# Kernel tuning notes

Measured on AMD Instinct MI355X. Metric: run time of the kernel, lower is better.

The kernel has to match this reference:

```python
import jax, jax.numpy as jnp
import numpy as np

BATCH, SEQ, H_IN, N_STATE, H_OUT = 16, 4096, 128, 256, 128
RMIN, RMAX, MAX_PHASE = 0.9, 1.0, 6.283


def setup_inputs() -> dict:
    key = jax.random.key(0)
    ks = jax.random.split(key, 9)
    u = jax.random.normal(ks[0], (BATCH, SEQ, H_IN), jnp.float32)
    # LRU exponential parameterization init (matches torch __init__)
    u1 = jax.random.uniform(ks[1], (N_STATE,), jnp.float32)
    u2 = jax.random.uniform(ks[2], (N_STATE,), jnp.float32)
    nu_log = jnp.log(-0.5 * jnp.log(u1 * (RMAX + RMIN) * (RMAX - RMIN) + RMIN ** 2))
    theta_log = jnp.log(MAX_PHASE * u2)
    lam_abs = jnp.exp(-jnp.exp(nu_log))
    gamma_log = jnp.log(jnp.sqrt(1.0 - lam_abs ** 2))
    s2in = np.sqrt(2.0 * H_IN).astype(np.float32)
    B_re = jax.random.normal(ks[3], (N_STATE, H_IN), jnp.float32) / s2in
    B_im = jax.random.normal(ks[4], (N_STATE, H_IN), jnp.float32) / s2in
    sst = np.sqrt(float(N_STATE)).astype(np.float32)
    C_re = jax.random.normal(ks[5], (H_OUT, N_STATE), jnp.float32) / sst
    C_im = jax.random.normal(ks[6], (H_OUT, N_STATE), jnp.float32) / sst
    D = jax.random.normal(ks[7], (H_OUT, H_IN), jnp.float32) / np.sqrt(float(H_IN)).astype(np.float32)
    return dict(u=u, nu_log=nu_log, theta_log=theta_log, gamma_log=gamma_log,
                B_re=B_re, B_im=B_im, C_re=C_re, C_im=C_im, D=D)


def _combine(a, b):
    # complex affine composition: (l, x) o (l', x') -> (l*l', l'*x + x')
    l1r, l1i, x1r, x1i = a
    l2r, l2i, x2r, x2i = b
    lr = l1r * l2r - l1i * l2i
    li = l1r * l2i + l1i * l2r
    xr = l2r * x1r - l2i * x1i + x2r
    xi = l2r * x1i + l2i * x1r + x2i
    return (lr, li, xr, xi)


def reference(u, nu_log, theta_log, gamma_log, B_re, B_im, C_re, C_im, D):
    lam_mod = jnp.exp(-jnp.exp(nu_log))          # |lambda|, [N]
    th = jnp.exp(theta_log)
    lam_re = lam_mod * jnp.cos(th)
    lam_im = lam_mod * jnp.sin(th)
    gammas = jnp.exp(gamma_log)                  # [N]
    # input projection Bu_t = gamma * (B @ u_t), complex -> real/imag parts
    Bu_re = jnp.einsum('blh,nh->bln', u, B_re) * gammas  # [B,L,N]
    Bu_im = jnp.einsum('blh,nh->bln', u, B_im) * gammas
    Bsz, L, N = Bu_re.shape
    lr = jnp.broadcast_to(lam_re, (Bsz, L, N))
    li = jnp.broadcast_to(lam_im, (Bsz, L, N))
    # parallel scan of x_t = lambda * x_{t-1} + Bu_t, x0 = 0
    _, _, xr, xi = jax.lax.associative_scan(_combine, (lr, li, Bu_re, Bu_im), axis=1)
    zero = jnp.zeros((Bsz, 1, N), u.dtype)
    pre_re = jnp.concatenate([zero, xr[:, :-1]], axis=1)  # states[:, :-1]
    pre_im = jnp.concatenate([zero, xi[:, :-1]], axis=1)
    # y_t = Re(C x_{t-1}) + D u_t
    y = (jnp.einsum('bln,on->blo', pre_re, C_re)
         - jnp.einsum('bln,on->blo', pre_im, C_im)
         + jnp.einsum('blh,oh->blo', u, D))
    return y
```

## Files before the change

### kernel.cpp

```cpp
#include <hip/hip_runtime.h>
#include <math.h>

#define BATCH 16
#define SEQ   4096
#define HIN   128
#define NST   256
#define HOUT  128
#define CL    32
#define NC    (SEQ/CL)
#define ROWS  (BATCH*SEQ)
#define KTOT  640
#define NPRE  512
#define NBU   512

typedef __attribute__((ext_vector_type(8))) short short8;
typedef __attribute__((ext_vector_type(4))) float f32x4;

__device__ inline unsigned short f2bf(float f) {
  union { float f; unsigned u; } v; v.f = f;
  unsigned r = v.u + 0x7FFFu + ((v.u >> 16) & 1u);
  return (unsigned short)(r >> 16);
}
__device__ inline float bf2f(unsigned short s) {
  union { unsigned u; float f; } v; v.u = ((unsigned)s) << 16;
  return v.f;
}

__global__ __launch_bounds__(256) void k_prep(
    const float* __restrict__ nu_log, const float* __restrict__ theta_log,
    const float* __restrict__ gamma_log,
    const float* __restrict__ Bre, const float* __restrict__ Bim,
    const float* __restrict__ Cre, const float* __restrict__ Cim,
    const float* __restrict__ Dm,
    float* __restrict__ lamre, float* __restrict__ lamim,
    unsigned short* __restrict__ Wb, unsigned short* __restrict__ W) {
  int idx = blockIdx.x*256 + threadIdx.x;
  if (idx < NST) {
    float lm = expf(-expf(nu_log[idx]));
    float th = expf(theta_log[idx]);
    lamre[idx] = lm * cosf(th);
    lamim[idx] = lm * sinf(th);
  }
  if (idx < 512*HIN) {
    int r = idx >> 7, h = idx & 127;
    int g = r >> 7;
    int w = r & 127;
    int n = g*64 + (w & 63);
    float gm = expf(gamma_log[n]);
    float v = (w < 64) ? Bre[n*HIN + h] : Bim[n*HIN + h];
    Wb[idx] = f2bf(gm * v);
  }
  if (idx < HOUT*KTOT) {
    int o = idx / KTOT, k = idx - o*KTOT;
    float v;
    if (k < NST)        v =  Cre[o*NST + k];
    else if (k < 2*NST) v = -Cim[o*NST + (k - NST)];
    else                v =  Dm[o*HIN + (k - 2*NST)];
    W[idx] = f2bf(v);
  }
}

__global__ __launch_bounds__(256) void k_cast(
    const float* __restrict__ u, unsigned short* __restrict__ ubf) {
  size_t i = (size_t)(blockIdx.x*256 + threadIdx.x) * 4;
  float4 v = *(const float4*)(u + i);
  ushort4 o;
  o.x = f2bf(v.x); o.y = f2bf(v.y); o.z = f2bf(v.z); o.w = f2bf(v.w);
  *(ushort4*)(ubf + i) = o;
}

union SharedBu {
  unsigned short B[128][136];
  float stg[2][32][132];
};
__global__ __launch_bounds__(256) void k_bu(
    const unsigned short* __restrict__ ubf, const unsigned short* __restrict__ Wb,
    const float* __restrict__ lamre, const float* __restrict__ lamim,
    unsigned short* __restrict__ bu16,
    float* __restrict__ S_re, float* __restrict__ S_im) {
  __shared__ unsigned short Asl[128][136];
  __shared__ SharedBu sh;
  int tid = threadIdx.x;
  int row0 = blockIdx.x * 128;
  int wid = tid >> 6, lane = tid & 63;
  int lm = lane & 15, lq = lane >> 4;
  int m0 = (wid >> 1) * 64, n0 = (wid & 1) * 64;
  int b = row0 >> 12;
  int cbase = (row0 & 4095) >> 5;
#pragma unroll
  for (int cc = 0; cc < 8; ++cc) {
    int ch = cc*256 + tid;
    int r = ch >> 4, h0 = (ch & 15) * 8;
    *(short8*)&Asl[r][h0] = *(const short8*)&ubf[(size_t)(row0 + r)*HIN + h0];
  }
  for (int g = 0; g < 4; ++g) {
    __syncthreads();
#pragma unroll
    for (int cc = 0; cc < 8; ++cc) {
      int ch = cc*256 + tid;
      int r = ch >> 4, h0 = (ch & 15) * 8;
      *(short8*)&sh.B[r][h0] = *(const short8*)&Wb[(size_t)(g*128 + r)*HIN + h0];
    }
    __syncthreads();
    f32x4 acc[4][4];
#pragma unroll
    for (int i = 0; i < 4; ++i)
#pragma unroll
      for (int j = 0; j < 4; ++j) acc[i][j] = (f32x4)0.f;
#pragma unroll
    for (int ks = 0; ks < 4; ++ks) {
      int k0 = ks*32 + lq*8;
      short8 a[4], bb[4];
#pragma unroll
      for (int i = 0; i < 4; ++i) a[i] = *(const short8*)&Asl[m0 + i*16 + lm][k0];
#pragma unroll
      for (int j = 0; j < 4; ++j) bb[j] = *(const short8*)&sh.B[n0 + j*16 + lm][k0];
#pragma unroll
      for (int i = 0; i < 4; ++i)
#pragma unroll
        for (int j = 0; j < 4; ++j)
          acc[i][j] = __builtin_amdgcn_mfma_f32_16x16x32_bf16(a[i], bb[j], acc[i][j], 0, 0, 0);
    }
#pragma unroll
    for (int i = 0; i < 4; ++i)
#pragma unroll
      for (int j = 0; j < 4; ++j)
#pragma unroll
        for (int r = 0; r < 4; ++r)
          bu16[(size_t)(row0 + m0 + i*16 + lq*4 + r)*NBU + g*128 + n0 + j*16 + lm] =
              f2bf(acc[i][j][r]);
    for (int p = 0; p < 2; ++p) {
      __syncthreads();
#pragma unroll
      for (int ii = 0; ii < 2; ++ii) {
        int i = 2*p + ii;
#pragma unroll
        for (int j = 0; j < 4; ++j)
#pragma unroll
          for (int r = 0; r < 4; ++r) {
            int trow = ii*16 + lq*4 + r;
            sh.stg[wid >> 1][trow][n0 + j*16 + lm] = acc[i][j][r];
          }
      }
      __syncthreads();
      if (tid < 128) {
        int buf = tid >> 6, nl = tid & 63;
        int ng = g*64 + nl;
        float lr = lamre[ng], li = lamim[ng];
        float sr = 0.f, si = 0.f;
#pragma unroll
        for (int t = 0; t < 32; ++t) {
          float br = sh.stg[buf][t][nl];
          float bi = sh.stg[buf][t][64 + nl];
          float nr = lr*sr - li*si + br;
          float ni = lr*si + li*sr + bi;
          sr = nr; si = ni;
        }
        int c = cbase + buf*2 + p;
        int idx = (b*NC + c)*NST + ng;
        S_re[idx] = sr; S_im[idx] = si;
      }
    }
  }
}

__global__ __launch_bounds__(256) void k_carry2(
    const float* __restrict__ S_re, const float* __restrict__ S_im,
    const float* __restrict__ lamre, const float* __restrict__ lamim,
    float* __restrict__ G_re, float* __restrict__ G_im) {
  int blk = blockIdx.x;
  int b = blk >> 3, g = blk & 7;
  int n = threadIdx.x;
  float ar = lamre[n], ai = lamim[n];
#pragma unroll
  for (int s = 0; s < 5; ++s) { float nr = ar*ar - ai*ai, ni = 2.f*ar*ai; ar = nr; ai = ni; }
  float tr = 0.f, ti = 0.f;
#pragma unroll
  for (int cc = 0; cc < 16; ++cc) {
    int idx = (b*NC + g*16 + cc)*NST + n;
    float nr = ar*tr - ai*ti + S_re[idx];
    float ni = ar*ti + ai*tr + S_im[idx];
    tr = nr; ti = ni;
  }
  int gi = (b*8 + g)*NST + n;
  G_re[gi] = tr; G_im[gi] = ti;
}

__global__ __launch_bounds__(256) void k_final(
    const float* __restrict__ S_re, const float* __restrict__ S_im,
    const float* __restrict__ G_re, const float* __restrict__ G_im,
    const float* __restrict__ lamre, const float* __restrict__ lamim,
    float* __restrict__ X0_re, float* __restrict__ X0_im) {
  int blk = blockIdx.x;
  int b = blk >> 3, g = blk & 7;
  int n = threadIdx.x;
  float ar = lamre[n], ai = lamim[n];
#pragma unroll
  for (int s = 0; s < 5; ++s) { float nr = ar*ar - ai*ai, ni = 2.f*ar*ai; ar = nr; ai = ni; }
  float a5r = ar, a5i = ai;
#pragma unroll
  for (int s = 0; s < 4; ++s) { float nr = a5r*a5r - a5i*a5i, ni = 2.f*a5r*a5i; a5r = nr; a5i = ni; }
  float pr = 0.f, pi = 0.f;
  for (int j = 0; j < g; ++j) {
    int gi = (b*8 + j)*NST + n;
    float nr = a5r*pr - a5i*pi + G_re[gi];
    float ni = a5r*pi + a5i*pr + G_im[gi];
    pr = nr; pi = ni;
  }
  float xr = pr, xi = pi;
#pragma unroll
  for (int cc = 0; cc < 16; ++cc) {
    int idx = (b*NC + g*16 + cc)*NST + n;
    X0_re[idx] = xr; X0_im[idx] = xi;
    float nr = ar*xr - ai*xi + S_re[idx];
    float ni = ar*xi + ai*xr + S_im[idx];
    xr = nr; xi = ni;
  }
}

__global__ __launch_bounds__(256) void k_scan(
    const unsigned short* __restrict__ bu16,
    const float* __restrict__ X0_re, const float* __restrict__ X0_im,
    const float* __restrict__ lamre, const float* __restrict__ lamim,
    unsigned short* __restrict__ pre16) {
  int blk = blockIdx.x;
  int b = blk >> 7, c = blk & (NC-1);
  int tid = threadIdx.x;
  int t0 = c*CL;
  size_t rowbase = (size_t)(b*SEQ + t0);
  int n = tid;
  int gg = n >> 6, nl = n & 63;
  int cre = gg*128 + nl, cim = cre + 64;
  const unsigned short* bup = bu16 + rowbase*NBU;
  unsigned short rbr[CL], rbi[CL];
#pragma unroll
  for (int t = 0; t < CL; ++t) {
    rbr[t] = bup[(size_t)t*NBU + cre];
    rbi[t] = bup[(size_t)t*NBU + cim];
  }
  float lr = lamre[n], li = lamim[n];
  int idx = (b*NC + c)*NST + n;
  float xr = X0_re[idx], xi = X0_im[idx];
  unsigned short* pdst = pre16 + rowbase*NPRE;
#pragma unroll
  for (int t = 0; t < CL; ++t) {
    pdst[n]       = f2bf(xr);
    pdst[NST + n] = f2bf(xi);
    float br = bf2f(rbr[t]);
    float bi = bf2f(rbi[t]);
    float nr = lr*xr - li*xi + br;
    float ni = lr*xi + li*xr + bi;
    xr = nr; xi = ni; pdst += NPRE;
  }
}

__global__ __launch_bounds__(256) void k_out2(
    const unsigned short* __restrict__ pre16, const unsigned short* __restrict__ ubf,
    const unsigned short* __restrict__ W, float* __restrict__ y) {
  __shared__ unsigned short Asl[128][136];
  __shared__ unsigned short Bsl[128][136];
  int tid = threadIdx.x;
  int row0 = blockIdx.x * 128;
  int wid = tid >> 6, lane = tid & 63;
  int lm = lane & 15, lq = lane >> 4;
  int m0 = (wid >> 1) * 64, n0 = (wid & 1) * 64;
  f32x4 acc[4][4];
#pragma unroll
  for (int i = 0; i < 4; ++i)
#pragma unroll
    for (int j = 0; j < 4; ++j) acc[i][j] = (f32x4)0.f;
  for (int s = 0; s < 5; ++s) {
#pragma unroll
    for (int cc = 0; cc < 8; ++cc) {
      int ch = cc*256 + tid;
      int r = ch >> 4, h0 = (ch & 15) * 8;
      if (s < 4)
        *(short8*)&Asl[r][h0] = *(const short8*)&pre16[(size_t)(row0 + r)*NPRE + s*128 + h0];
      else
        *(short8*)&Asl[r][h0] = *(const short8*)&ubf[(size_t)(row0 + r)*HIN + h0];
      *(short8*)&Bsl[r][h0] = *(const short8*)&W[(size_t)r*KTOT + s*128 + h0];
    }
    __syncthreads();
#pragma unroll
    for (int ks = 0; ks < 4; ++ks) {
      int k0 = ks*32 + lq*8;
      short8 a[4], bb[4];
#pragma unroll
      for (int i = 0; i < 4; ++i) a[i] = *(const short8*)&Asl[m0 + i*16 + lm][k0];
#pragma unroll
      for (int j = 0; j < 4; ++j) bb[j] = *(const short8*)&Bsl[n0 + j*16 + lm][k0];
#pragma unroll
      for (int i = 0; i < 4; ++i)
#pragma unroll
        for (int j = 0; j < 4; ++j)
          acc[i][j] = __builtin_amdgcn_mfma_f32_16x16x32_bf16(a[i], bb[j], acc[i][j], 0, 0, 0);
    }
    __syncthreads();
  }
#pragma unroll
  for (int i = 0; i < 4; ++i)
#pragma unroll
    for (int j = 0; j < 4; ++j)
#pragma unroll
      for (int r = 0; r < 4; ++r)
        y[(size_t)(row0 + m0 + i*16 + lq*4 + r)*HOUT + n0 + j*16 + lm] = acc[i][j][r];
}

extern "C" void kernel_launch(void* const* d_in, const int* in_sizes, int n_in,
                              void* d_out, int out_size, void* d_ws, size_t ws_size,
                              hipStream_t stream) {
  const float* u         = (const float*)d_in[0];
  const float* nu_log    = (const float*)d_in[1];
  const float* theta_log = (const float*)d_in[2];
  const float* gamma_log = (const float*)d_in[3];
  const float* B_re      = (const float*)d_in[4];
  const float* B_im      = (const float*)d_in[5];
  const float* C_re      = (const float*)d_in[6];
  const float* C_im      = (const float*)d_in[7];
  const float* Dm        = (const float*)d_in[8];
  float* y = (float*)d_out;
  char* ws = (char*)d_ws;

  float*          lamre = (float*)(ws);
  float*          lamim = (float*)(ws + 1024);
  unsigned short* ubf   = (unsigned short*)(ws + 4096);
  unsigned short* Wb    = (unsigned short*)(ws + 4096 + 16777216);
  unsigned short* W     = (unsigned short*)(ws + 4096 + 16777216 + 131072);
  unsigned short* bu16  = (unsigned short*)(ws + 4096 + 16777216 + 131072 + 163840);
  char* pp = ws + 4096 + 16777216 + 131072 + 163840 + (size_t)ROWS*NBU*2;
  unsigned short* pre16 = (unsigned short*)pp;
  char* p2 = pp + (size_t)ROWS*NPRE*2;
  float* S_re  = (float*)(p2);
  float* S_im  = (float*)(p2 + 2097152);
  float* G_re  = (float*)(p2 + 2*2097152);
  float* G_im  = (float*)(p2 + 2*2097152 + 131072);
  float* X0_re = (float*)(p2 + 2*2097152 + 2*131072);
  float* X0_im = (float*)(p2 + 3*2097152 + 2*131072);

  k_prep<<<320, 256, 0, stream>>>(nu_log, theta_log, gamma_log, B_re, B_im,
                                  C_re, C_im, Dm, lamre, lamim, Wb, W);
  k_cast<<<(ROWS*HIN)/1024, 256, 0, stream>>>(u, ubf);
  k_bu<<<ROWS/128, 256, 0, stream>>>(ubf, Wb, lamre, lamim, bu16, S_re, S_im);
  k_carry2<<<BATCH*8, 256, 0, stream>>>(S_re, S_im, lamre, lamim, G_re, G_im);
  k_final<<<BATCH*8, 256, 0, stream>>>(S_re, S_im, G_re, G_im, lamre, lamim,
                                       X0_re, X0_im);
  k_scan<<<BATCH*NC, 256, 0, stream>>>(bu16, X0_re, X0_im, lamre, lamim, pre16);
  k_out2<<<ROWS/128, 256, 0, stream>>>(pre16, ubf, W, y);
}
```

Baseline: 187.9 us.

## Fuse chunk-local scan into Bu GEMM and apply carry correction in output GEMM

The chunk-local scan states (starting from zero) are now written as bf16 directly from the Bu GEMM kernel, which removes the bu16 buffer and the separate k_scan kernel. The output GEMM adds the carry term lambda^j * X0 while loading its A tile, using a precomputed table of lambda powers built in k_prep. This saves one full read and write of a large intermediate plus one kernel launch. In exchange, the output GEMM's load path does more global loads and arithmetic, and k_bu issues scattered 2-byte stores from only 128 threads.

```diff
diff --git a/kernel.cpp b/kernel.cpp
--- a/kernel.cpp
+++ b/kernel.cpp
@@ -11,7 +11,6 @@
 #define ROWS  (BATCH*SEQ)
 #define KTOT  640
 #define NPRE  512
-#define NBU   512
 
 typedef __attribute__((ext_vector_type(8))) short short8;
 typedef __attribute__((ext_vector_type(4))) float f32x4;
@@ -33,13 +32,22 @@
     const float* __restrict__ Cre, const float* __restrict__ Cim,
     const float* __restrict__ Dm,
     float* __restrict__ lamre, float* __restrict__ lamim,
+    float* __restrict__ lamPowRe, float* __restrict__ lamPowIm,
     unsigned short* __restrict__ Wb, unsigned short* __restrict__ W) {
   int idx = blockIdx.x*256 + threadIdx.x;
   if (idx < NST) {
     float lm = expf(-expf(nu_log[idx]));
     float th = expf(theta_log[idx]);
-    lamre[idx] = lm * cosf(th);
-    lamim[idx] = lm * sinf(th);
+    float lr = lm * cosf(th), li = lm * sinf(th);
+    lamre[idx] = lr; lamim[idx] = li;
+    float pr = 1.f, pi = 0.f;
+    for (int j = 0; j < CL; ++j) {
+      lamPowRe[j*NST + idx] = pr;
+      lamPowIm[j*NST + idx] = pi;
+      float nr = pr*lr - pi*li;
+      float ni = pr*li + pi*lr;
+      pr = nr; pi = ni;
+    }
   }
   if (idx < 512*HIN) {
     int r = idx >> 7, h = idx & 127;
@@ -76,7 +84,7 @@
 __global__ __launch_bounds__(256) void k_bu(
     const unsigned short* __restrict__ ubf, const unsigned short* __restrict__ Wb,
     const float* __restrict__ lamre, const float* __restrict__ lamim,
-    unsigned short* __restrict__ bu16,
+    unsigned short* __restrict__ preL,
     float* __restrict__ S_re, float* __restrict__ S_im) {
   __shared__ unsigned short Asl[128][136];
   __shared__ SharedBu sh;
@@ -121,14 +129,6 @@
         for (int j = 0; j < 4; ++j)
           acc[i][j] = __builtin_amdgcn_mfma_f32_16x16x32_bf16(a[i], bb[j], acc[i][j], 0, 0, 0);
     }
-#pragma unroll
-    for (int i = 0; i < 4; ++i)
-#pragma unroll
-      for (int j = 0; j < 4; ++j)
-#pragma unroll
-        for (int r = 0; r < 4; ++r)
-          bu16[(size_t)(row0 + m0 + i*16 + lq*4 + r)*NBU + g*128 + n0 + j*16 + lm] =
-              f2bf(acc[i][j][r]);
     for (int p = 0; p < 2; ++p) {
       __syncthreads();
 #pragma unroll
@@ -147,14 +147,22 @@
         int buf = tid >> 6, nl = tid & 63;
         int ng = g*64 + nl;
         float lr = lamre[ng], li = lamim[ng];
+        float rr[CL], ri[CL];
+#pragma unroll
+        for (int t = 0; t < CL; ++t) {
+          rr[t] = sh.stg[buf][t][nl];
+          ri[t] = sh.stg[buf][t][64 + nl];
+        }
+        int rowb = row0 + buf*64 + p*32;
+        unsigned short* pl = preL + (size_t)rowb*NPRE;
         float sr = 0.f, si = 0.f;
 #pragma unroll
-        for (int t = 0; t < 32; ++t) {
-          float br = sh.stg[buf][t][nl];
-          float bi = sh.stg[buf][t][64 + nl];
-          float nr = lr*sr - li*si + br;
-          float ni = lr*si + li*sr + bi;
-          sr = nr; si = ni;
+        for (int t = 0; t < CL; ++t) {
+          pl[ng]       = f2bf(sr);
+          pl[NST + ng] = f2bf(si);
+          float nr = lr*sr - li*si + rr[t];
+          float ni = lr*si + li*sr + ri[t];
+          sr = nr; si = ni; pl += NPRE;
         }
         int c = cbase + buf*2 + p;
         int idx = (b*NC + c)*NST + ng;
@@ -218,45 +226,12 @@
   }
 }
 
-__global__ __launch_bounds__(256) void k_scan(
-    const unsigned short* __restrict__ bu16,
+__global__ __launch_bounds__(256) void k_out2(
+    const unsigned short* __restrict__ preL, const unsigned short* __restrict__ ubf,
+    const unsigned short* __restrict__ W,
+    const float* __restrict__ lamPowRe, const float* __restrict__ lamPowIm,
     const float* __restrict__ X0_re, const float* __restrict__ X0_im,
-    const float* __restrict__ lamre, const float* __restrict__ lamim,
-    unsigned short* __restrict__ pre16) {
-  int blk = blockIdx.x;
-  int b = blk >> 7, c = blk & (NC-1);
-  int tid = threadIdx.x;
-  int t0 = c*CL;
-  size_t rowbase = (size_t)(b*SEQ + t0);
-  int n = tid;
-  int gg = n >> 6, nl = n & 63;
-  int cre = gg*128 + nl, cim = cre + 64;
-  const unsigned short* bup = bu16 + rowbase*NBU;
-  unsigned short rbr[CL], rbi[CL];
-#pragma unroll
-  for (int t = 0; t < CL; ++t) {
-    rbr[t] = bup[(size_t)t*NBU + cre];
-    rbi[t] = bup[(size_t)t*NBU + cim];
-  }
-  float lr = lamre[n], li = lamim[n];
-  int idx = (b*NC + c)*NST + n;
-  float xr = X0_re[idx], xi = X0_im[idx];
-  unsigned short* pdst = pre16 + rowbase*NPRE;
-#pragma unroll
-  for (int t = 0; t < CL; ++t) {
-    pdst[n]       = f2bf(xr);
-    pdst[NST + n] = f2bf(xi);
-    float br = bf2f(rbr[t]);
-    float bi = bf2f(rbi[t]);
-    float nr = lr*xr - li*xi + br;
-    float ni = lr*xi + li*xr + bi;
-    xr = nr; xi = ni; pdst += NPRE;
-  }
-}
-
-__global__ __launch_bounds__(256) void k_out2(
-    const unsigned short* __restrict__ pre16, const unsigned short* __restrict__ ubf,
-    const unsigned short* __restrict__ W, float* __restrict__ y) {
+    float* __restrict__ y) {
   __shared__ unsigned short Asl[128][136];
   __shared__ unsigned short Bsl[128][136];
   int tid = threadIdx.x;
@@ -274,10 +249,32 @@
     for (int cc = 0; cc < 8; ++cc) {
       int ch = cc*256 + tid;
       int r = ch >> 4, h0 = (ch & 15) * 8;
-      if (s < 4)
-        *(short8*)&Asl[r][h0] = *(const short8*)&pre16[(size_t)(row0 + r)*NPRE + s*128 + h0];
-      else
+      if (s < 4) {
+        int row = row0 + r;
+        int j = row & 31, cidx = row >> 5;
+        int n = ((s & 1) << 7) + h0;
+        short8 loc = *(const short8*)&preL[(size_t)row*NPRE + s*128 + h0];
+        float lre[8], lim_[8], x0r[8], x0i[8];
+        *(float4*)&lre[0]  = *(const float4*)&lamPowRe[j*NST + n];
+        *(float4*)&lre[4]  = *(const float4*)&lamPowRe[j*NST + n + 4];
+        *(float4*)&lim_[0] = *(const float4*)&lamPowIm[j*NST + n];
+        *(float4*)&lim_[4] = *(const float4*)&lamPowIm[j*NST + n + 4];
+        *(float4*)&x0r[0]  = *(const float4*)&X0_re[cidx*NST + n];
+        *(float4*)&x0r[4]  = *(const float4*)&X0_re[cidx*NST + n + 4];
+        *(float4*)&x0i[0]  = *(const float4*)&X0_im[cidx*NST + n];
+        *(float4*)&x0i[4]  = *(const float4*)&X0_im[cidx*NST + n + 4];
+        unsigned short o[8];
+#pragma unroll
+        for (int e = 0; e < 8; ++e) {
+          float lv = bf2f((unsigned short)loc[e]);
+          float v = (s < 2) ? (lv + lre[e]*x0r[e] - lim_[e]*x0i[e])
+                            : (lv + lre[e]*x0i[e] + lim_[e]*x0r[e]);
+          o[e] = f2bf(v);
+        }
+        *(short8*)&Asl[r][h0] = *(const short8*)o;
+      } else {
         *(short8*)&Asl[r][h0] = *(const short8*)&ubf[(size_t)(row0 + r)*HIN + h0];
+      }
       *(short8*)&Bsl[r][h0] = *(const short8*)&W[(size_t)r*KTOT + s*128 + h0];
     }
     __syncthreads();
@@ -321,15 +318,15 @@
   float* y = (float*)d_out;
   char* ws = (char*)d_ws;
 
-  float*          lamre = (float*)(ws);
-  float*          lamim = (float*)(ws + 1024);
-  unsigned short* ubf   = (unsigned short*)(ws + 4096);
-  unsigned short* Wb    = (unsigned short*)(ws + 4096 + 16777216);
-  unsigned short* W     = (unsigned short*)(ws + 4096 + 16777216 + 131072);
-  unsigned short* bu16  = (unsigned short*)(ws + 4096 + 16777216 + 131072 + 163840);
-  char* pp = ws + 4096 + 16777216 + 131072 + 163840 + (size_t)ROWS*NBU*2;
-  unsigned short* pre16 = (unsigned short*)pp;
-  char* p2 = pp + (size_t)ROWS*NPRE*2;
+  float*          lamre    = (float*)(ws);
+  float*          lamim    = (float*)(ws + 1024);
+  float*          lamPowRe = (float*)(ws + 4096);
+  float*          lamPowIm = (float*)(ws + 4096 + 32768);
+  unsigned short* ubf      = (unsigned short*)(ws + 69632);
+  unsigned short* Wb       = (unsigned short*)(ws + 69632 + 16777216);
+  unsigned short* W        = (unsigned short*)(ws + 69632 + 16777216 + 131072);
+  unsigned short* preL     = (unsigned short*)(ws + 69632 + 16777216 + 131072 + 163840);
+  char* p2 = ws + 69632 + 16777216 + 131072 + 163840 + (size_t)ROWS*NPRE*2;
   float* S_re  = (float*)(p2);
   float* S_im  = (float*)(p2 + 2097152);
   float* G_re  = (float*)(p2 + 2*2097152);
@@ -338,12 +335,13 @@
   float* X0_im = (float*)(p2 + 3*2097152 + 2*131072);
 
   k_prep<<<320, 256, 0, stream>>>(nu_log, theta_log, gamma_log, B_re, B_im,
-                                  C_re, C_im, Dm, lamre, lamim, Wb, W);
+                                  C_re, C_im, Dm, lamre, lamim,
+                                  lamPowRe, lamPowIm, Wb, W);
   k_cast<<<(ROWS*HIN)/1024, 256, 0, stream>>>(u, ubf);
-  k_bu<<<ROWS/128, 256, 0, stream>>>(ubf, Wb, lamre, lamim, bu16, S_re, S_im);
+  k_bu<<<ROWS/128, 256, 0, stream>>>(ubf, Wb, lamre, lamim, preL, S_re, S_im);
   k_carry2<<<BATCH*8, 256, 0, stream>>>(S_re, S_im, lamre, lamim, G_re, G_im);
   k_final<<<BATCH*8, 256, 0, stream>>>(S_re, S_im, G_re, G_im, lamre, lamim,
                                        X0_re, X0_im);
-  k_scan<<<BATCH*NC, 256, 0, stream>>>(bu16, X0_re, X0_im, lamre, lamim, pre16);
-  k_out2<<<ROWS/128, 256, 0, stream>>>(pre16, ubf, W, y);
-}
+  k_out2<<<ROWS/128, 256, 0, stream>>>(preL, ubf, W, lamPowRe, lamPowIm,
+                                       X0_re, X0_im, y);
+}
```

Result: faster. 181.0 us (-3.6%).
